# Performance work log

Measured on AMD Instinct MI355X. Metric: run time of the kernel, lower is better.

## Reference

```python
import jax, jax.numpy as jnp
import numpy as np
import math

LN_EPS = 1e-5

def _ln(x, g, b):
    m = jnp.mean(x, -1, keepdims=True)
    v = jnp.mean((x - m) ** 2, -1, keepdims=True)
    return (x - m) / jnp.sqrt(v + LN_EPS) * g + b

def setup_inputs() -> dict:
    key = jax.random.key(0)
    ks = jax.random.split(key, 16)
    B, N, D, V = 2, 512, 128, 16
    w = lambda k, shape: jax.random.normal(k, shape, jnp.float32) * 0.02
    return {
        "scalar": jax.random.normal(ks[0], (B, N, D), jnp.float32),
        "vector": jax.random.normal(ks[1], (B, N, 3, V), jnp.float32),
        "coords": jax.random.normal(ks[2], (B, N, 3), jnp.float32),
        "w_q": w(ks[3], (D, D)), "b_q": jnp.zeros((D,), jnp.float32),
        "w_k": w(ks[4], (D, D)), "b_k": jnp.zeros((D,), jnp.float32),
        "w_v": w(ks[5], (D, D)), "b_v": jnp.zeros((D,), jnp.float32),
        "w_d1": w(ks[6], (1, D)), "b_d1": jnp.zeros((D,), jnp.float32),
        "w_d2": w(ks[7], (D, D)), "b_d2": jnp.zeros((D,), jnp.float32),
        "w_g": w(ks[8], (D, V)), "b_g": jnp.zeros((V,), jnp.float32),
        "w_o": w(ks[9], (D, D)), "b_o": jnp.zeros((D,), jnp.float32),
        "w_f1": w(ks[10], (D, 2 * D)), "b_f1": jnp.zeros((2 * D,), jnp.float32),
        "w_f2": w(ks[11], (2 * D, D)), "b_f2": jnp.zeros((D,), jnp.float32),
        "w_vo": w(ks[12], (V, V)), "b_vo": jnp.zeros((V,), jnp.float32),
        "g_s": jnp.ones((D,), jnp.float32), "be_s": jnp.zeros((D,), jnp.float32),
        "g_v": jnp.ones((V,), jnp.float32), "be_v": jnp.zeros((V,), jnp.float32),
    }

def reference(scalar, vector, coords, w_q, b_q, w_k, b_k, w_v, b_v,
              w_d1, b_d1, w_d2, b_d2, w_g, b_g, w_o, b_o,
              w_f1, b_f1, w_f2, b_f2, w_vo, b_vo, g_s, be_s, g_v, be_v):
    D = scalar.shape[-1]
    # pairwise geometry: [B,N,N,3], [B,N,N,1]
    rel = coords[:, :, None, :] - coords[:, None, :, :]
    dist = jnp.linalg.norm(rel, axis=-1, keepdims=True)
    direction = rel / jnp.maximum(dist, 1e-6)
    sn = _ln(scalar, g_s, be_s)
    q = sn @ w_q + b_q
    k = sn @ w_k + b_k
    v = sn @ w_v + b_v
    # distance-conditioned bias: [B,N,N,D]
    bias = jax.nn.gelu(dist @ w_d1 + b_d1, approximate=False) @ w_d2 + b_d2
    # q_i . (k_j + bias_ij) / sqrt(D)
    logits = (jnp.einsum('bid,bjd->bij', q, k)
              + jnp.einsum('bid,bijd->bij', q, bias)) / math.sqrt(D)
    attn = jax.nn.softmax(logits, axis=-1)
    # sum_j attn_ij * (v_j + bias_ij)
    upd = jnp.einsum('bij,bjd->bid', attn, v) + jnp.einsum('bij,bijd->bid', attn, bias)
    scalar = scalar + (upd @ w_o + b_o)
    h = _ln(scalar, g_s, be_s)
    scalar = scalar + (jax.nn.gelu(h @ w_f1 + b_f1, approximate=False) @ w_f2 + b_f2)
    gate = jax.nn.sigmoid(scalar @ w_g + b_g)  # [B,N,V]
    # sum_j attn_ij * (vector_j + dir_ij * gate_i) decomposed (same math, no BxNxNx3xV tensor)
    agg = (jnp.einsum('bij,bjcv->bicv', attn, vector)
           + jnp.einsum('bij,bijc->bic', attn, direction)[..., None] * gate[:, :, None, :])
    projected = _ln(agg, g_v, be_v) @ w_vo + b_vo
    return scalar, vector + projected
```

## Files before the change

### kernel.cpp

```cpp
#include <hip/hip_runtime.h>
#include <math.h>

#define D 128
#define F 256
#define V 16
#define NSEQ 512
#define NROW 1024
#define MQ 7

typedef unsigned short u16;

__device__ __forceinline__ float gelu_exact(float x) {
    return 0.5f * x * (1.0f + erff(x * 0.70710678118654752f));
}
__device__ __forceinline__ float bf2f(u16 u) {
    return __uint_as_float(((unsigned)u) << 16);
}
__device__ __forceinline__ u16 f2bf(float x) {
    unsigned u = __float_as_uint(x);
    u += 0x7fffu + ((u >> 16) & 1u);
    return (u16)(u >> 16);
}

__device__ __forceinline__ float waveSum(float v) {
#pragma unroll
    for (int o = 32; o; o >>= 1) v += __shfl_xor(v, o);
    return v;
}
__device__ __forceinline__ float waveMax(float v) {
#pragma unroll
    for (int o = 32; o; o >>= 1) v = fmaxf(v, __shfl_xor(v, o));
    return v;
}

__device__ __forceinline__ void build_A(const float* __restrict__ w_d1,
                                        const float* __restrict__ b_d1,
                                        float* A_s, int t) {
    if (t < D) {
        const float gam[MQ] = {0.f, 0.5f, 0.39894228f, 0.f, -0.06649038f, 0.f,
                               0.0099735570f};
        float w = w_d1[t], b = b_d1[t];
        float wp[MQ], bp[MQ];
        wp[0] = 1.f; bp[0] = 1.f;
#pragma unroll
        for (int i = 1; i < MQ; i++) { wp[i] = wp[i - 1] * w; bp[i] = bp[i - 1] * b; }
        float A[MQ];
#pragma unroll
        for (int m = 0; m < MQ; m++) A[m] = 0.f;
#pragma unroll
        for (int k = 1; k < MQ; k++) {
            float g = gam[k];
            if (g == 0.f) continue;
            float C = 1.f;
            for (int m = 0; m <= k; m++) {
                A[m] = fmaf(g * C, wp[m] * bp[k - m], A[m]);
                C = C * (float)(k - m) / (float)(m + 1);
            }
        }
#pragma unroll
        for (int m = 0; m < MQ; m++) A_s[t * MQ + m] = A[m];
    }
}

__global__ __launch_bounds__(1024, 8) void k1_qkv(
    const float* __restrict__ scalar, const float* __restrict__ vecin,
    const float* __restrict__ w_q, const float* __restrict__ b_q,
    const float* __restrict__ w_k, const float* __restrict__ b_k,
    const float* __restrict__ w_v, const float* __restrict__ b_v,
    const float* __restrict__ w_d1, const float* __restrict__ b_d1,
    const float* __restrict__ w_d2,
    const float* __restrict__ w_o, const float* __restrict__ w_f1,
    const float* __restrict__ w_f2, const float* __restrict__ w_g,
    const float* __restrict__ g_s, const float* __restrict__ be_s,
    float* __restrict__ qg, u16* __restrict__ kTh, u16* __restrict__ vh,
    u16* __restrict__ wobf, u16* __restrict__ wf1bf, u16* __restrict__ wf2bf,
    u16* __restrict__ wgbf, u16* __restrict__ vinbf,
    float* __restrict__ Gg)
{
    const int t = threadIdx.x, l = t & 127, h2 = (t >> 7) & 1;
    const int wvid = t >> 6, ln = t & 63;
    const int r0 = blockIdx.x * 2, r = r0 + h2;
    __shared__ __align__(8) float snT[D][2];
    __shared__ float k_s[2][D];
    __shared__ float A_s[D * MQ];
    __shared__ float P3[3][8][2][D];
    __shared__ float redA[16], redB[16];

    {
        const unsigned idx = blockIdx.x * 1024u + (unsigned)t;
        if (idx < 16384u)       wobf[idx] = f2bf(w_o[idx]);
        else if (idx < 49152u)  wf1bf[idx - 16384u] = f2bf(w_f1[idx - 16384u]);
        else if (idx < 81920u)  wf2bf[idx - 49152u] = f2bf(w_f2[idx - 49152u]);
        else if (idx < 83968u)  wgbf[idx - 81920u] = f2bf(w_g[idx - 81920u]);
        else if (idx < 133120u) vinbf[idx - 83968u] = f2bf(vecin[idx - 83968u]);
    }

    float x = scalar[(size_t)r * D + l];
    { float s = waveSum(x); if (ln == 0) redA[wvid] = s; }
    __syncthreads();
    float mean = 0.f;
#pragma unroll
    for (int dd = 0; dd < 4; dd++) mean += redA[4 * dd + 2 * h2] + redA[4 * dd + 2 * h2 + 1];
    mean *= (1.0f / 512.0f);
    float dv = x - mean;
    { float s = waveSum(dv * dv); if (ln == 0) redB[wvid] = s; }
    __syncthreads();
    float var = 0.f;
#pragma unroll
    for (int dd = 0; dd < 4; dd++) var += redB[4 * dd + 2 * h2] + redB[4 * dd + 2 * h2 + 1];
    var *= (1.0f / 512.0f);
    if (t < 256) snT[l][h2] = dv * rsqrtf(var + 1e-5f) * g_s[l] + be_s[l];
    __syncthreads();

    {
        const int eo = t >> 7, e0 = eo * 16;
        float aq0 = 0.f, aq1 = 0.f, ak0 = 0.f, ak1 = 0.f, av0 = 0.f, av1 = 0.f;
#pragma unroll 4
        for (int e = e0; e < e0 + 16; e++) {
            float2 s2 = *(const float2*)&snT[e][0];
            float wq = w_q[e * D + l], wk = w_k[e * D + l], wv = w_v[e * D + l];
            aq0 = fmaf(s2.x, wq, aq0); aq1 = fmaf(s2.y, wq, aq1);
            ak0 = fmaf(s2.x, wk, ak0); ak1 = fmaf(s2.y, wk, ak1);
            av0 = fmaf(s2.x, wv, av0); av1 = fmaf(s2.y, wv, av1);
        }
        P3[0][eo][0][l] = aq0; P3[0][eo][1][l] = aq1;
        P3[1][eo][0][l] = ak0; P3[1][eo][1][l] = ak1;
        P3[2][eo][0][l] = av0; P3[2][eo][1][l] = av1;
    }
    __syncthreads();

    if (t < 768) {
        const int mat = t >> 8, h3 = (t >> 7) & 1, l2 = t & 127;
        float acc = 0.f;
#pragma unroll
        for (int eo = 0; eo < 8; eo++) acc += P3[mat][eo][h3][l2];
        if (mat == 0)      qg[(size_t)(r0 + h3) * D + l2] = acc + b_q[l2];
        else if (mat == 1) k_s[h3][l2] = acc + b_k[l2];
        else               vh[(size_t)(r0 + h3) * D + l2] = f2bf(acc + b_v[l2]);
    }
    __syncthreads();
    if (t < 256) kTh[(size_t)(t >> 1) * NROW + r0 + (t & 1)] = f2bf(k_s[t & 1][t >> 1]);

    if (blockIdx.x == 0) {
        build_A(w_d1, b_d1, A_s, t);
        __syncthreads();
        if (t < D * MQ) {
            const int m = t >> 7, l2 = t & 127;
            float acc = 0.f;
#pragma unroll 4
            for (int e = 0; e < D; e++)
                acc = fmaf(w_d2[e * D + l2], A_s[e * MQ + m], acc);
            Gg[l2 * MQ + m] = acc;
        }
    }
}

__global__ __launch_bounds__(1024, 8) void k23(
    const float* __restrict__ coords, const float* __restrict__ vecin,
    const float* __restrict__ scalar,
    const float* __restrict__ qg, const u16* __restrict__ kTh,
    const u16* __restrict__ vh, const float* __restrict__ Gg,
    const float* __restrict__ b_d2,
    const u16* __restrict__ wobf, const float* __restrict__ b_o,
    const u16* __restrict__ wf1bf, const float* __restrict__ b_f1,
    const u16* __restrict__ wf2bf, const float* __restrict__ b_f2,
    const u16* __restrict__ wgbf, const float* __restrict__ b_g,
    const u16* __restrict__ vinbf,
    const float* __restrict__ w_vo, const float* __restrict__ b_vo,
    const float* __restrict__ g_s, const float* __restrict__ be_s,
    const float* __restrict__ g_v, const float* __restrict__ be_v,
    float* __restrict__ out_s, float* __restrict__ out_v)
{
    const int t = threadIdx.x, wvid = t >> 6, ln = t & 63;
    const int r0 = blockIdx.x * 2, b = blockIdx.x >> 8;
    __shared__ __align__(16) float RA[5632];
    __shared__ __align__(8) float qT[D][2];
    __shared__ float Gl[D * MQ];
    __shared__ float P_s[2][MQ];
    __shared__ __align__(8) float updT[D][2], hT[D][2], s1T[D][2];
    __shared__ __align__(8) float t2T[F][2];
    __shared__ float S_s[2][MQ], adir_s[2][3], avec_s[2][48];
    __shared__ float redA[16], redB[16], wredM[16][10];
    __shared__ float gate_s[2][V], gp[8][2][V], lnv_s[2][48];

    if (t < 256) qT[t & 127][t >> 7] = qg[(size_t)(r0 + (t >> 7)) * D + (t & 127)];
    if (t < D * MQ) Gl[t] = Gg[t];
    __syncthreads();

    {
        const int dd = t & 127, hp = (t >> 7) & 1;
        float qv = qT[dd][hp];
        float pa[MQ];
#pragma unroll
        for (int m = 0; m < MQ; m++) pa[m] = qv * Gl[dd * MQ + m];
        pa[0] = fmaf(qv, b_d2[dd], pa[0]);
#pragma unroll
        for (int m = 0; m < MQ; m++) {
            float s = waveSum(pa[m]);
            if (ln == 0) wredM[wvid][m] = s;
        }
    }
    __syncthreads();
    if (t < 2 * MQ) {
        const int hh = t / MQ, m = t % MQ;
        float s = 0.f;
#pragma unroll
        for (int dd = 0; dd < 4; dd++)
            s += wredM[4 * dd + 2 * hh][m] + wredM[4 * dd + 2 * hh + 1][m];
        P_s[hh][m] = s * 0.25f;
    }

    {
        const int jj = t & 511, eh = t >> 9;
        const u16* ke = kTh + (size_t)(64 * eh) * NROW + (size_t)b * NSEQ + jj;
        float c0 = 0.f, c1 = 0.f;
#pragma unroll 8
        for (int e = 0; e < 64; e++) {
            float kv = bf2f(ke[(size_t)e * NROW]);
            float2 q2 = *(const float2*)&qT[64 * eh + e][0];
            c0 = fmaf(q2.x, kv, c0);
            c1 = fmaf(q2.y, kv, c1);
        }
        *(float2*)&RA[2048 + (eh * 512 + jj) * 2] = make_float2(c0, c1);
    }
    __syncthreads();

    const int h2 = t >> 9, j = t & 511, r = r0 + h2;
    const float cix = coords[(size_t)r * 3 + 0];
    const float ciy = coords[(size_t)r * 3 + 1];
    const float ciz = coords[(size_t)r * 3 + 2];
    const float* cj = coords + ((size_t)b * NSEQ + j) * 3;
    float rx = cix - cj[0], ry = ciy - cj[1], rz = ciz - cj[2];
    float dj = sqrtf(rx * rx + ry * ry + rz * rz);
    float qk = RA[2048 + j * 2 + h2] + RA[2048 + (512 + j) * 2 + h2];
    float Pr[MQ];
#pragma unroll
    for (int m = 0; m < MQ; m++) Pr[m] = P_s[h2][m];
    float bias = Pr[MQ - 1];
#pragma unroll
    for (int m = MQ - 2; m >= 0; m--) bias = fmaf(bias, dj, Pr[m]);
    const float sc = 0.08838834764831844f;
    float lg = (qk + bias) * sc;

    { float mx = waveMax(lg); if (ln == 0) redA[wvid] = mx; }
    __syncthreads();
    float mx = redA[8 * h2];
#pragma unroll
    for (int k = 1; k < 8; k++) mx = fmaxf(mx, redA[8 * h2 + k]);
    float p = __expf(lg - mx);
    { float s = waveSum(p); if (ln == 0) redB[wvid] = s; }
    __syncthreads();
    float lsum = 0.f;
#pragma unroll
    for (int k = 0; k < 8; k++) lsum += redB[8 * h2 + k];
    float a = p / lsum;
    RA[j * 2 + h2] = a;

    {
        float red[10];
        float w0 = a;
#pragma unroll
        for (int m = 0; m < MQ; m++) { red[m] = w0; w0 *= dj; }
        float ia = a * __builtin_amdgcn_rcpf(fmaxf(dj, 1e-6f));
        red[7] = ia * rx; red[8] = ia * ry; red[9] = ia * rz;
#pragma unroll
        for (int m = 0; m < 10; m++) {
            float s = waveSum(red[m]);
            if (ln == 0) wredM[wvid][m] = s;
        }
    }
    __syncthreads();
    if (t < 20) {
        const int hh = t / 10, m = t % 10;
        float s = 0.f;
#pragma unroll
        for (int k = 0; k < 8; k++) s += wredM[8 * hh + k][m];
        if (m < MQ) S_s[hh][m] = s;
        else        adir_s[hh][m - MQ] = s;
    }

    {
        const int dd = t & 127, jo = t >> 7, jb = 64 * jo;
        const u16* vb = vh + ((size_t)b * NSEQ + jb) * D + dd;
        float c0 = 0.f, c1 = 0.f;
#pragma unroll 8
        for (int jj = 0; jj < 64; jj++) {
            float2 at = *(const float2*)&RA[(jb + jj) * 2];
            float vv = bf2f(vb[(size_t)jj * D]);
            c0 = fmaf(at.x, vv, c0);
            c1 = fmaf(at.y, vv, c1);
        }
        RA[2048 + (jo * 2 + 0) * 128 + dd] = c0;
        RA[2048 + (jo * 2 + 1) * 128 + dd] = c1;
    }
    if (ln < 48) {
        const int jb = 32 * wvid;
        const u16* vp = vinbf + ((size_t)b * NSEQ + jb) * 48 + ln;
        float c0 = 0.f, c1 = 0.f;
#pragma unroll 4
        for (int jj = 0; jj < 32; jj++) {
            float2 at = *(const float2*)&RA[(jb + jj) * 2];
            float vv = bf2f(vp[(size_t)jj * 48]);
            c0 = fmaf(at.x, vv, c0);
            c1 = fmaf(at.y, vv, c1);
        }
        RA[4096 + (wvid * 2 + 0) * 48 + ln] = c0;
        RA[4096 + (wvid * 2 + 1) * 48 + ln] = c1;
    }
    __syncthreads();

    if (t < 256) {
        const int hh = t >> 7, l = t & 127;
        float acc = 0.f;
#pragma unroll
        for (int jo = 0; jo < 8; jo++) acc += RA[2048 + (jo * 2 + hh) * 128 + l];
        float aa = 0.f;
#pragma unroll
        for (int m = 0; m < MQ; m++) aa = fmaf(Gl[l * MQ + m], S_s[hh][m], aa);
        updT[l][hh] = acc + aa + b_d2[l];
    } else if (t - 256 < 96) {
        const int idx = t - 256, hh = idx / 48, i2 = idx % 48;
        float s = 0.f;
#pragma unroll
        for (int w2 = 0; w2 < 16; w2++) s += RA[4096 + (w2 * 2 + hh) * 48 + i2];
        avec_s[hh][i2] = s;
    }
    __syncthreads();

    {
        const int eo = t >> 7, l = t & 127, e0 = 16 * eo;
        float c0 = 0.f, c1 = 0.f;
#pragma unroll 4
        for (int e = e0; e < e0 + 16; e++) {
            float2 up = *(const float2*)&updT[e][0];
            float wv = bf2f(wobf[e * D + l]);
            c0 = fmaf(up.x, wv, c0);
            c1 = fmaf(up.y, wv, c1);
        }
        RA[2048 + (eo * 2 + 0) * 128 + l] = c0;
        RA[2048 + (eo * 2 + 1) * 128 + l] = c1;
    }
    __syncthreads();
    float xln = 0.f;
    {
        const int hh = (t >> 7) & 1, l = t & 127;
        if (t < 256) {
            float acc = 0.f;
#pragma unroll
            for (int eo = 0; eo < 8; eo++) acc += RA[2048 + (eo * 2 + hh) * 128 + l];
            xln = scalar[(size_t)(r0 + hh) * D + l] + acc + b_o[l];
            s1T[l][hh] = xln;
        }
        float s = waveSum(xln);
        if (t < 256 && ln == 0) redA[wvid] = s;
    }
    __syncthreads();
    float dvv = 0.f;
    if (t < 256) {
        const int hh = (t >> 7) & 1;
        float mean = (redA[2 * hh] + redA[2 * hh + 1]) * (1.0f / 128.0f);
        dvv = xln - mean;
    }
    {
        float s = waveSum(dvv * dvv);
        if (t < 256 && ln == 0) redB[wvid] = s;
    }
    __syncthreads();
    if (t < 256) {
        const int hh = (t >> 7) & 1, l = t & 127;
        float var = (redB[2 * hh] + redB[2 * hh + 1]) * (1.0f / 128.0f);
        hT[l][hh] = dvv * rsqrtf(var + 1e-5f) * g_s[l] + be_s[l];
    }
    __syncthreads();

    {
        const int f = t & 255, eq = t >> 8, e0 = 32 * eq;
        float c0 = 0.f, c1 = 0.f;
#pragma unroll 4
        for (int e = e0; e < e0 + 32; e++) {
            float2 hv = *(const float2*)&hT[e][0];
            float wv = bf2f(wf1bf[e * F + f]);
            c0 = fmaf(hv.x, wv, c0);
            c1 = fmaf(hv.y, wv, c1);
        }
        RA[2048 + (eq * 2 + 0) * 256 + f] = c0;
        RA[2048 + (eq * 2 + 1) * 256 + f] = c1;
    }
    __syncthreads();
    if (t < 512) {
        const int hh = t >> 8, f = t & 255;
        float acc = 0.f;
#pragma unroll
        for (int eq = 0; eq < 4; eq++) acc += RA[2048 + (eq * 2 + hh) * 256 + f];
        t2T[f][hh] = gelu_exact(acc + b_f1[f]);
    }
    __syncthreads();

    {
        const int fo = t >> 7, l = t & 127, f0 = 32 * fo;
        float c0 = 0.f, c1 = 0.f;
#pragma unroll 4
        for (int f = f0; f < f0 + 32; f++) {
            float2 tv = *(const float2*)&t2T[f][0];
            float wv = bf2f(wf2bf[f * D + l]);
            c0 = fmaf(tv.x, wv, c0);
            c1 = fmaf(tv.y, wv, c1);
        }
        RA[2048 + (fo * 2 + 0) * 128 + l] = c0;
        RA[2048 + (fo * 2 + 1) * 128 + l] = c1;
    }
    __syncthreads();
    if (t < 256) {
        const int hh = t >> 7, l = t & 127;
        float acc = 0.f;
#pragma unroll
        for (int fo = 0; fo < 8; fo++) acc += RA[2048 + (fo * 2 + hh) * 128 + l];
        float v2 = s1T[l][hh] + acc + b_f2[l];
        out_s[(size_t)(r0 + hh) * D + l] = v2;
        s1T[l][hh] = v2;
    }
    __syncthreads();

    if (t < 256) {
        const int dq = t >> 5, rr = (t >> 4) & 1, vv = t & 15, d0 = 16 * dq;
        float aa = 0.f;
#pragma unroll 4
        for (int dd = d0; dd < d0 + 16; dd++)
            aa = fmaf(s1T[dd][rr], bf2f(wgbf[dd * V + vv]), aa);
        gp[dq][rr][vv] = aa;
    }
    __syncthreads();
    if (t < 32) {
        const int rr = t >> 4, vv = t & 15;
        float aa = b_g[vv];
#pragma unroll
        for (int dq = 0; dq < 8; dq++) aa += gp[dq][rr][vv];
        gate_s[rr][vv] = 1.0f / (1.0f + __expf(-aa));
    }
    __syncthreads();

    if (t < 96) {
        const int rr = t / 48, idx = t % 48, c = idx >> 4, vv = idx & 15;
        float agg = avec_s[rr][idx] + adir_s[rr][c] * gate_s[rr][vv];
        float s = agg;
#pragma unroll
        for (int o = 8; o; o >>= 1) s += __shfl_xor(s, o, 16);
        float mean = s * (1.0f / 16.0f);
        float e = agg - mean;
        float s2 = e * e;
#pragma unroll
        for (int o = 8; o; o >>= 1) s2 += __shfl_xor(s2, o, 16);
        float rstd = rsqrtf(s2 * (1.0f / 16.0f) + 1e-5f);
        lnv_s[rr][idx] = e * rstd * g_v[vv] + be_v[vv];
    }
    __syncthreads();
    if (t < 96) {
        const int rr = t / 48, idx = t % 48, c = idx >> 4, vv = idx & 15;
        const int row = r0 + rr;
        float aa = b_vo[vv];
#pragma unroll
        for (int w2 = 0; w2 < V; w2++)
            aa = fmaf(lnv_s[rr][c * V + w2], w_vo[w2 * V + vv], aa);
        out_v[(size_t)row * 48 + idx] = vecin[(size_t)row * 48 + idx] + aa;
    }
}

extern "C" void kernel_launch(void* const* d_in, const int* in_sizes, int n_in,
                              void* d_out, int out_size, void* d_ws, size_t ws_size,
                              hipStream_t stream)
{
    (void)in_sizes; (void)n_in; (void)out_size; (void)ws_size;
    const float* scalar = (const float*)d_in[0];
    const float* vecin  = (const float*)d_in[1];
    const float* coords = (const float*)d_in[2];
    const float* w_q  = (const float*)d_in[3];  const float* b_q  = (const float*)d_in[4];
    const float* w_k  = (const float*)d_in[5];  const float* b_k  = (const float*)d_in[6];
    const float* w_v  = (const float*)d_in[7];  const float* b_v  = (const float*)d_in[8];
    const float* w_d1 = (const float*)d_in[9];  const float* b_d1 = (const float*)d_in[10];
    const float* w_d2 = (const float*)d_in[11]; const float* b_d2 = (const float*)d_in[12];
    const float* w_g  = (const float*)d_in[13]; const float* b_g  = (const float*)d_in[14];
    const float* w_o  = (const float*)d_in[15]; const float* b_o  = (const float*)d_in[16];
    const float* w_f1 = (const float*)d_in[17]; const float* b_f1 = (const float*)d_in[18];
    const float* w_f2 = (const float*)d_in[19]; const float* b_f2 = (const float*)d_in[20];
    const float* w_vo = (const float*)d_in[21]; const float* b_vo = (const float*)d_in[22];
    const float* g_s  = (const float*)d_in[23]; const float* be_s = (const float*)d_in[24];
    const float* g_v  = (const float*)d_in[25]; const float* be_v = (const float*)d_in[26];

    float* ws = (float*)d_ws;
    float* qg    = ws;
    u16*   kTh   = (u16*)(ws + 131072);
    u16*   vh    = kTh + 131072;
    u16*   wobf  = vh + 131072;
    u16*   wf1bf = wobf + 16384;
    u16*   wf2bf = wf1bf + 32768;
    u16*   wgbf  = wf2bf + 32768;
    u16*   vinbf = wgbf + 2048;
    float* Gg    = (float*)(vinbf + 49152);

    float* out_s = (float*)d_out;
    float* out_v = out_s + 131072;

    hipLaunchKernelGGL(k1_qkv, dim3(NROW / 2), dim3(1024), 0, stream,
                       scalar, vecin, w_q, b_q, w_k, b_k, w_v, b_v, w_d1, b_d1,
                       w_d2, w_o, w_f1, w_f2, w_g, g_s, be_s,
                       qg, kTh, vh, wobf, wf1bf, wf2bf, wgbf, vinbf, Gg);
    hipLaunchKernelGGL(k23, dim3(NROW / 2), dim3(1024), 0, stream,
                       coords, vecin, scalar, qg, kTh, vh, Gg,
                       b_d2, wobf, b_o, wf1bf, b_f1, wf2bf, b_f2,
                       wgbf, b_g, vinbf, w_vo, b_vo, g_s, be_s, g_v, be_v,
                       out_s, out_v);
}
```

Measured before the change: 160.5 us.

## Process four rows per block in QKV kernel and defer softmax normalization

```diff
diff --git a/kernel.cpp b/kernel.cpp
--- a/kernel.cpp
+++ b/kernel.cpp
@@ -77,13 +77,13 @@
     u16* __restrict__ wgbf, u16* __restrict__ vinbf,
     float* __restrict__ Gg)
 {
-    const int t = threadIdx.x, l = t & 127, h2 = (t >> 7) & 1;
+    const int t = threadIdx.x, l = t & 127, h = (t >> 7) & 3;
     const int wvid = t >> 6, ln = t & 63;
-    const int r0 = blockIdx.x * 2, r = r0 + h2;
-    __shared__ __align__(8) float snT[D][2];
-    __shared__ float k_s[2][D];
+    const int r0 = blockIdx.x * 4, r = r0 + h;
+    __shared__ __align__(16) float snT[D][4];
+    __shared__ float k_s[4][D];
     __shared__ float A_s[D * MQ];
-    __shared__ float P3[3][8][2][D];
+    __shared__ float P3[3][8][4][D];
     __shared__ float redA[16], redB[16];
 
     {
@@ -98,39 +98,41 @@
     float x = scalar[(size_t)r * D + l];
     { float s = waveSum(x); if (ln == 0) redA[wvid] = s; }
     __syncthreads();
-    float mean = 0.f;
-#pragma unroll
-    for (int dd = 0; dd < 4; dd++) mean += redA[4 * dd + 2 * h2] + redA[4 * dd + 2 * h2 + 1];
-    mean *= (1.0f / 512.0f);
+    float mean = (redA[2 * h] + redA[2 * h + 1]
+                + redA[8 + 2 * h] + redA[8 + 2 * h + 1]) * (1.0f / 256.0f);
     float dv = x - mean;
     { float s = waveSum(dv * dv); if (ln == 0) redB[wvid] = s; }
     __syncthreads();
-    float var = 0.f;
-#pragma unroll
-    for (int dd = 0; dd < 4; dd++) var += redB[4 * dd + 2 * h2] + redB[4 * dd + 2 * h2 + 1];
-    var *= (1.0f / 512.0f);
-    if (t < 256) snT[l][h2] = dv * rsqrtf(var + 1e-5f) * g_s[l] + be_s[l];
+    float var = (redB[2 * h] + redB[2 * h + 1]
+               + redB[8 + 2 * h] + redB[8 + 2 * h + 1]) * (1.0f / 256.0f);
+    if (t < 512) snT[l][h] = dv * rsqrtf(var + 1e-5f) * g_s[l] + be_s[l];
     __syncthreads();
 
     {
         const int eo = t >> 7, e0 = eo * 16;
-        float aq0 = 0.f, aq1 = 0.f, ak0 = 0.f, ak1 = 0.f, av0 = 0.f, av1 = 0.f;
+        float aq[4] = {0, 0, 0, 0}, ak[4] = {0, 0, 0, 0}, av[4] = {0, 0, 0, 0};
 #pragma unroll 4
         for (int e = e0; e < e0 + 16; e++) {
-            float2 s2 = *(const float2*)&snT[e][0];
+            float4 s4 = *(const float4*)&snT[e][0];
             float wq = w_q[e * D + l], wk = w_k[e * D + l], wv = w_v[e * D + l];
-            aq0 = fmaf(s2.x, wq, aq0); aq1 = fmaf(s2.y, wq, aq1);
-            ak0 = fmaf(s2.x, wk, ak0); ak1 = fmaf(s2.y, wk, ak1);
-            av0 = fmaf(s2.x, wv, av0); av1 = fmaf(s2.y, wv, av1);
-        }
-        P3[0][eo][0][l] = aq0; P3[0][eo][1][l] = aq1;
-        P3[1][eo][0][l] = ak0; P3[1][eo][1][l] = ak1;
-        P3[2][eo][0][l] = av0; P3[2][eo][1][l] = av1;
-    }
-    __syncthreads();
-
-    if (t < 768) {
-        const int mat = t >> 8, h3 = (t >> 7) & 1, l2 = t & 127;
+            aq[0] = fmaf(s4.x, wq, aq[0]); aq[1] = fmaf(s4.y, wq, aq[1]);
+            aq[2] = fmaf(s4.z, wq, aq[2]); aq[3] = fmaf(s4.w, wq, aq[3]);
+            ak[0] = fmaf(s4.x, wk, ak[0]); ak[1] = fmaf(s4.y, wk, ak[1]);
+            ak[2] = fmaf(s4.z, wk, ak[2]); ak[3] = fmaf(s4.w, wk, ak[3]);
+            av[0] = fmaf(s4.x, wv, av[0]); av[1] = fmaf(s4.y, wv, av[1]);
+            av[2] = fmaf(s4.z, wv, av[2]); av[3] = fmaf(s4.w, wv, av[3]);
+        }
+#pragma unroll
+        for (int rr = 0; rr < 4; rr++) {
+            P3[0][eo][rr][l] = aq[rr];
+            P3[1][eo][rr][l] = ak[rr];
+            P3[2][eo][rr][l] = av[rr];
+        }
+    }
+    __syncthreads();
+
+    for (int idx = t; idx < 1536; idx += 1024) {
+        const int mat = idx >> 9, h3 = (idx >> 7) & 3, l2 = idx & 127;
         float acc = 0.f;
 #pragma unroll
         for (int eo = 0; eo < 8; eo++) acc += P3[mat][eo][h3][l2];
@@ -139,7 +141,7 @@
         else               vh[(size_t)(r0 + h3) * D + l2] = f2bf(acc + b_v[l2]);
     }
     __syncthreads();
-    if (t < 256) kTh[(size_t)(t >> 1) * NROW + r0 + (t & 1)] = f2bf(k_s[t & 1][t >> 1]);
+    if (t < 512) kTh[(size_t)(t >> 2) * NROW + r0 + (t & 3)] = f2bf(k_s[t & 3][t >> 2]);
 
     if (blockIdx.x == 0) {
         build_A(w_d1, b_d1, A_s, t);
@@ -179,8 +181,8 @@
     __shared__ float P_s[2][MQ];
     __shared__ __align__(8) float updT[D][2], hT[D][2], s1T[D][2];
     __shared__ __align__(8) float t2T[F][2];
-    __shared__ float S_s[2][MQ], adir_s[2][3], avec_s[2][48];
-    __shared__ float redA[16], redB[16], wredM[16][10];
+    __shared__ float S_s[2][MQ], adir_s[2][3], avec_s[2][48], inv_s[2];
+    __shared__ float redA[16], wredM[16][10];
     __shared__ float gate_s[2][V], gp[8][2][V], lnv_s[2][48];
 
     if (t < 256) qT[t & 127][t >> 7] = qg[(size_t)(r0 + (t >> 7)) * D + (t & 127)];
@@ -248,21 +250,15 @@
 #pragma unroll
     for (int k = 1; k < 8; k++) mx = fmaxf(mx, redA[8 * h2 + k]);
     float p = __expf(lg - mx);
-    { float s = waveSum(p); if (ln == 0) redB[wvid] = s; }
-    __syncthreads();
-    float lsum = 0.f;
-#pragma unroll
-    for (int k = 0; k < 8; k++) lsum += redB[8 * h2 + k];
-    float a = p / lsum;
-    RA[j * 2 + h2] = a;
+    RA[j * 2 + h2] = p;
 
     {
         float red[10];
-        float w0 = a;
+        float w0 = p;
 #pragma unroll
         for (int m = 0; m < MQ; m++) { red[m] = w0; w0 *= dj; }
-        float ia = a * __builtin_amdgcn_rcpf(fmaxf(dj, 1e-6f));
-        red[7] = ia * rx; red[8] = ia * ry; red[9] = ia * rz;
+        float ip = p * __builtin_amdgcn_rcpf(fmaxf(dj, 1e-6f));
+        red[7] = ip * rx; red[8] = ip * ry; red[9] = ip * rz;
 #pragma unroll
         for (int m = 0; m < 10; m++) {
             float s = waveSum(red[m]);
@@ -270,13 +266,23 @@
         }
     }
     __syncthreads();
+    {
+        float lsum = 0.f;
+#pragma unroll
+        for (int k = 0; k < 8; k++) lsum += wredM[8 * h2 + k][0];
+        if ((t & 511) == 0) inv_s[h2] = 1.0f / lsum;
+    }
     if (t < 20) {
         const int hh = t / 10, m = t % 10;
+        float lsum = 0.f;
+#pragma unroll
+        for (int k = 0; k < 8; k++) lsum += wredM[8 * hh + k][0];
+        float inv = 1.0f / lsum;
         float s = 0.f;
 #pragma unroll
         for (int k = 0; k < 8; k++) s += wredM[8 * hh + k][m];
-        if (m < MQ) S_s[hh][m] = s;
-        else        adir_s[hh][m - MQ] = s;
+        if (m < MQ) S_s[hh][m] = s * inv;
+        else        adir_s[hh][m - MQ] = s * inv;
     }
 
     {
@@ -317,13 +323,13 @@
         float aa = 0.f;
 #pragma unroll
         for (int m = 0; m < MQ; m++) aa = fmaf(Gl[l * MQ + m], S_s[hh][m], aa);
-        updT[l][hh] = acc + aa + b_d2[l];
+        updT[l][hh] = acc * inv_s[hh] + aa + b_d2[l];
     } else if (t - 256 < 96) {
         const int idx = t - 256, hh = idx / 48, i2 = idx % 48;
         float s = 0.f;
 #pragma unroll
         for (int w2 = 0; w2 < 16; w2++) s += RA[4096 + (w2 * 2 + hh) * 48 + i2];
-        avec_s[hh][i2] = s;
+        avec_s[hh][i2] = s * inv_s[hh];
     }
     __syncthreads();
 
@@ -363,12 +369,12 @@
     }
     {
         float s = waveSum(dvv * dvv);
-        if (t < 256 && ln == 0) redB[wvid] = s;
+        if (t < 256 && ln == 0) redA[wvid + 8] = s;
     }
     __syncthreads();
     if (t < 256) {
         const int hh = (t >> 7) & 1, l = t & 127;
-        float var = (redB[2 * hh] + redB[2 * hh + 1]) * (1.0f / 128.0f);
+        float var = (redA[8 + 2 * hh] + redA[8 + 2 * hh + 1]) * (1.0f / 128.0f);
         hT[l][hh] = dvv * rsqrtf(var + 1e-5f) * g_s[l] + be_s[l];
     }
     __syncthreads();
@@ -500,7 +506,7 @@
     float* out_s = (float*)d_out;
     float* out_v = out_s + 131072;
 
-    hipLaunchKernelGGL(k1_qkv, dim3(NROW / 2), dim3(1024), 0, stream,
+    hipLaunchKernelGGL(k1_qkv, dim3(NROW / 4), dim3(1024), 0, stream,
                        scalar, vecin, w_q, b_q, w_k, b_k, w_v, b_v, w_d1, b_d1,
                        w_d2, w_o, w_f1, w_f2, w_g, g_s, be_s,
                        qg, kTh, vh, wobf, wf1bf, wf2bf, wgbf, vinbf, Gg);
```

Measured after the change: 159.5 us. No clear change (-0.6%).
